# Kernel optimization log

Measured on AMD Instinct MI355X. Metric: run time of the kernel, lower is better.

Reference implementation:

```python
import jax, jax.numpy as jnp
import numpy as np

N = 100000   # nodes
E = 800000   # edges
D = 16       # embedding_dimension
H = 128      # hidden_dimension
O = 3        # out_dim
R = 2        # relation_num
SLOPE = 0.01 # torch LeakyReLU default negative_slope


def setup_inputs() -> dict:
    key = jax.random.key(0)
    ks = jax.random.split(key, 16)
    s = 0.05
    return {
        "mask_feature": jax.random.normal(ks[0], (N, D), jnp.float32),
        "feature": jax.random.normal(ks[1], (N, D), jnp.float32),
        "W1": jax.random.normal(ks[2], (D, H), jnp.float32) * s,
        "b1": jax.random.normal(ks[3], (H,), jnp.float32) * s,
        "rg1_w": jax.random.normal(ks[4], (R, H, H), jnp.float32) * s,
        "rg1_root": jax.random.normal(ks[5], (H, H), jnp.float32) * s,
        "rg1_b": jax.random.normal(ks[6], (H,), jnp.float32) * s,
        "rg2_w": jax.random.normal(ks[7], (R, H, H), jnp.float32) * s,
        "rg2_root": jax.random.normal(ks[8], (H, H), jnp.float32) * s,
        "rg2_b": jax.random.normal(ks[9], (H,), jnp.float32) * s,
        "Wo": jax.random.normal(ks[10], (H, O), jnp.float32) * s,
        "bo": jax.random.normal(ks[11], (O,), jnp.float32) * s,
        "edge_index": jax.random.randint(ks[12], (2, E), 0, N, jnp.int64),
        "edge_type": jax.random.randint(ks[13], (E,), 0, R, jnp.int64),
    }


def _rgcn_conv(x, src, dst, w_rel, w_root, bias):
    """PyG RGCNConv with default mean aggregation per relation + root + bias."""
    out = x @ w_root + bias                      # [N, H] root/self term
    xj = x[src]                                  # [E, H] gather source features
    for r in range(R):
        rmask = _EDGE_TYPE_MASKS[r]              # [E] bool, edge_type == r
        msg = jnp.where(rmask[:, None], xj @ w_rel[r], 0.0)   # [E, H]
        agg = jax.ops.segment_sum(msg, dst, num_segments=N)   # [N, H]
        cnt = jax.ops.segment_sum(rmask.astype(x.dtype), dst, num_segments=N)
        out = out + agg / jnp.maximum(cnt, 1.0)[:, None]       # mean aggr
    return out


_EDGE_TYPE_MASKS = None


def reference(mask_feature, feature, W1, b1, rg1_w, rg1_root, rg1_b,
              rg2_w, rg2_root, rg2_b, Wo, bo, edge_index, edge_type):
    global _EDGE_TYPE_MASKS
    src, dst = edge_index[0], edge_index[1]
    _EDGE_TYPE_MASKS = [edge_type == r for r in range(R)]

    def branch(inp):
        h = jax.nn.leaky_relu(inp @ W1 + b1, SLOPE)      # linear_relu_input
        h = _rgcn_conv(h, src, dst, rg1_w, rg1_root, rg1_b)
        # dropout: identity in eval mode
        h = _rgcn_conv(h, src, dst, rg2_w, rg2_root, rg2_b)
        return h @ Wo + bo                               # linear_output [N, O]

    x = branch(mask_feature.astype(jnp.float32))
    mask = branch(feature - mask_feature)
    return x * mask                                      # [N, O]
```

## Files before the change

kernel.cpp:

```cpp
#include <hip/hip_runtime.h>
#include <hip/hip_fp16.h>

#define Nn 100000
#define Ee 800000
#define Dd 16
#define Hh 128
#define Oo 3
#define Rr 2
#define HROW 256
#define Mm (Rr * Nn)
#define CNTB4 ((Ee + 1023) / 1024)
#define SWB 48
#define INTB ((Nn + 127) / 128)
#define NT_IN 128
#define FN 16
#define MPAD 516
#define OPAD 264

typedef _Float16 half8 __attribute__((ext_vector_type(8)));
typedef _Float16 half4 __attribute__((ext_vector_type(4)));
typedef float floatx4 __attribute__((ext_vector_type(4)));

__global__ void k_diag(float* out, float v) { out[0] = v; }

__global__ __launch_bounds__(256) void k_prep_all(
    const int* __restrict__ ei, const int* __restrict__ et,
    int* __restrict__ cnt, int* __restrict__ eidx, int cap,
    const float* __restrict__ r1root, const float* __restrict__ r1w,
    const float* __restrict__ r2root, const float* __restrict__ r2w,
    __half* __restrict__ Bsw1, __half* __restrict__ Bsw2,
    const float* __restrict__ mf, const float* __restrict__ ff,
    const float* __restrict__ W1, const float* __restrict__ b1,
    __half* __restrict__ H) {
    int tid = threadIdx.x;
    int bx = blockIdx.x;

    if (bx < INTB) {
        int n0 = bx * NT_IN;
        int j = tid & 127;
        int hf = __builtin_amdgcn_readfirstlane(tid >> 7);
        float wk[Dd];
#pragma unroll
        for (int k = 0; k < Dd; ++k) wk[k] = W1[k * Hh + j];
        float bj = b1[j];
        int nbeg = n0 + hf * 64;
        int nend = nbeg + 64;
        if (nend > Nn) nend = Nn;
#pragma unroll 2
        for (int n = nbeg; n < nend; ++n) {
            const float* xr = mf + (size_t)n * Dd;
            const float* fr = ff + (size_t)n * Dd;
            float a0 = bj, a1 = bj;
#pragma unroll
            for (int k = 0; k < Dd; ++k) {
                float xv = xr[k];
                float fv = fr[k];
                a0 = fmaf(xv, wk[k], a0);
                a1 = fmaf(fv, wk[k], a1);
                a1 = fmaf(-xv, wk[k], a1);
            }
            a0 = a0 > 0.f ? a0 : 0.01f * a0;
            a1 = a1 > 0.f ? a1 : 0.01f * a1;
            H[(size_t)n * HROW + j] = __float2half(a0);
            H[(size_t)n * HROW + Hh + j] = __float2half(a1);
        }
        return;
    }
    int sb = bx - INTB;
    if (sb < CNTB4) {
        int e0 = (sb * 256 + tid) * 4;
        if (e0 < Ee) {
            int4 s4 = *(const int4*)(ei + e0);
            int4 d4 = *(const int4*)(ei + Ee + e0);
            int4 t4 = *(const int4*)(et + e0);
            int gb, pos;
            gb = t4.x * Nn + d4.x; pos = atomicAdd(&cnt[gb], 1);
            if (pos < cap) eidx[(size_t)gb * cap + pos] = s4.x;
            gb = t4.y * Nn + d4.y; pos = atomicAdd(&cnt[gb], 1);
            if (pos < cap) eidx[(size_t)gb * cap + pos] = s4.y;
            gb = t4.z * Nn + d4.z; pos = atomicAdd(&cnt[gb], 1);
            if (pos < cap) eidx[(size_t)gb * cap + pos] = s4.z;
            gb = t4.w * Nn + d4.w; pos = atomicAdd(&cnt[gb], 1);
            if (pos < cap) eidx[(size_t)gb * cap + pos] = s4.w;
        }
        return;
    }
    sb -= CNTB4;
    {
        const float* wroot = (sb < 24) ? r1root : r2root;
        const float* wrel = (sb < 24) ? r1w : r2w;
        __half* Bsw = (sb < 24) ? Bsw1 : Bsw2;
        int idx = (sb % 24) * 256 + tid;
        if (idx >= 8 * 12 * 64) return;
        int l = idx & 63;
        int s = (idx >> 6) % 12;
        int t = (idx >> 6) / 12;
        int n = (l & 15) * 8 + t;
        int k0 = s * 32 + (l >> 4) * 8;
        __half tmp[8];
#pragma unroll
        for (int jj = 0; jj < 8; ++jj) {
            int k = k0 + jj;
            float v = (k < Hh) ? wroot[k * Hh + n] : wrel[(size_t)(k - Hh) * Hh + n];
            tmp[jj] = __float2half(v);
        }
        *(uint4*)(Bsw + (size_t)idx * 8) = *(uint4*)tmp;
    }
}

__global__ __launch_bounds__(256, 6) void k_conv_f(const __half* __restrict__ Hin,
                                                   __half* __restrict__ Hout,
                                                   const int* __restrict__ cnt,
                                                   const int* __restrict__ eidx, int cap,
                                                   const __half* __restrict__ Bsw,
                                                   const float* __restrict__ bias,
                                                   const __half* __restrict__ zrow,
                                                   int do_final,
                                                   const float* __restrict__ Wo,
                                                   const float* __restrict__ bo,
                                                   float* __restrict__ out) {
    __shared__ __align__(16) char smem[FN * MPAD * 2];
    __shared__ float WoS[Hh * Oo];
    __shared__ float bS[Oo];
    auto TM = (__half(*)[MPAD])smem;
    auto TO = (__half(*)[OPAD])smem;

    int tid = threadIdx.x;
    int n0 = blockIdx.x * FN;
    int wv = tid >> 6;
    int lane = tid & 63;

    if (do_final) {
        for (int i = tid; i < Hh * Oo; i += 256) WoS[i] = Wo[i];
        if (tid < Oo) bS[tid] = bo[tid];
    }

    int hh32 = lane >> 5;
    int sl = lane & 31;
    const __half* zr = zrow + sl * 8;

    int cn0[4], cn1[4], sidx[4];
#pragma unroll
    for (int p = 0; p < 4; ++p) {
        int gb0 = n0 + wv * 4 + p;
        cn0[p] = cnt[gb0];
        cn1[p] = cnt[gb0 + Nn];
        sidx[p] = eidx[(size_t)(hh32 * Nn + gb0) * cap + sl];
    }

#pragma unroll
    for (int p = 0; p < 4; ++p) {
        int nl = wv * 4 + p;
        int cn_h = hh32 ? cn1[p] : cn0[p];
        int len = cn_h < 32 ? cn_h : 32;
        int mlr = cn0[p] > cn1[p] ? cn0[p] : cn1[p];
        int maxlen = mlr < 32 ? mlr : 32;

        int bc[8];
#pragma unroll
        for (int u = 0; u < 8; ++u) bc[u] = __shfl(sidx[p], u, 32);

        float2 ac[4];
#pragma unroll
        for (int j = 0; j < 4; ++j) { ac[j].x = 0.f; ac[j].y = 0.f; }

        {
            half8 v0 = *(const half8*)(const void*)((0 < len) ? Hin + (size_t)bc[0] * HROW + sl * 8 : zr);
            half8 v1 = *(const half8*)(const void*)((1 < len) ? Hin + (size_t)bc[1] * HROW + sl * 8 : zr);
            half8 v2 = *(const half8*)(const void*)((2 < len) ? Hin + (size_t)bc[2] * HROW + sl * 8 : zr);
            half8 v3 = *(const half8*)(const void*)((3 < len) ? Hin + (size_t)bc[3] * HROW + sl * 8 : zr);
            half8 s = (v0 + v1) + (v2 + v3);
#pragma unroll
            for (int j = 0; j < 4; ++j) {
                ac[j].x += (float)s[2 * j];
                ac[j].y += (float)s[2 * j + 1];
            }
        }
        if (maxlen > 4) {
            half8 v0 = *(const half8*)(const void*)((4 < len) ? Hin + (size_t)bc[4] * HROW + sl * 8 : zr);
            half8 v1 = *(const half8*)(const void*)((5 < len) ? Hin + (size_t)bc[5] * HROW + sl * 8 : zr);
            half8 v2 = *(const half8*)(const void*)((6 < len) ? Hin + (size_t)bc[6] * HROW + sl * 8 : zr);
            half8 v3 = *(const half8*)(const void*)((7 < len) ? Hin + (size_t)bc[7] * HROW + sl * 8 : zr);
            half8 s = (v0 + v1) + (v2 + v3);
#pragma unroll
            for (int j = 0; j < 4; ++j) {
                ac[j].x += (float)s[2 * j];
                ac[j].y += (float)s[2 * j + 1];
            }
            if (maxlen > 8) {
                for (int e = 8; e < maxlen; e += 4) {
                    half8 v[4];
#pragma unroll
                    for (int u = 0; u < 4; ++u) {
                        int s_ = __shfl(sidx[p], e + u, 32);
                        v[u] = *(const half8*)(const void*)(
                            ((e + u) < len) ? Hin + (size_t)s_ * HROW + sl * 8 : zr);
                    }
                    half8 s2 = (v[0] + v[1]) + (v[2] + v[3]);
#pragma unroll
                    for (int j = 0; j < 4; ++j) {
                        ac[j].x += (float)s2[2 * j];
                        ac[j].y += (float)s2[2 * j + 1];
                    }
                }
            }
        }

        float iv = 1.0f / fmaxf((float)cn_h, 1.0f);
        __half2 o[4];
#pragma unroll
        for (int j = 0; j < 4; ++j)
            o[j] = __floats2half2_rn(ac[j].x * iv, ac[j].y * iv);
        __half* dst = &TM[nl][hh32 * 256 + sl * 8];
        *(uint2*)dst = *(uint2*)&o[0];
        *(uint2*)(dst + 4) = *(uint2*)&o[2];
    }
    __syncthreads();

    int b = wv >> 1;
    int hh = wv & 1;
    int quad = lane >> 4;
    int l15 = lane & 15;

    floatx4 acc[4];
#pragma unroll
    for (int t = 0; t < 4; ++t) {
        float bv = bias[l15 * 8 + hh * 4 + t];
        acc[t][0] = bv; acc[t][1] = bv; acc[t][2] = bv; acc[t][3] = bv;
    }

    const __half* hrow = Hin + (size_t)(n0 + l15) * HROW + b * Hh + quad * 8;
#pragma unroll
    for (int s = 0; s < 12; ++s) {
        half8 af;
        if (s < 4)
            af = *(const half8*)(const void*)(hrow + s * 32);
        else
            af = *(const half8*)(const void*)&TM[l15][((s >> 2) - 1) * 256 + b * 128 +
                                                     (s & 3) * 32 + quad * 8];
#pragma unroll
        for (int t = 0; t < 4; ++t) {
            half8 bf = *(const half8*)(const void*)(
                Bsw + ((size_t)((hh * 4 + t) * 12 + s) * 64 + lane) * 8);
            acc[t] = __builtin_amdgcn_mfma_f32_16x16x32_f16(af, bf, acc[t], 0, 0, 0);
        }
    }

    if (!do_final) {
#pragma unroll
        for (int r = 0; r < 4; ++r) {
            int node = n0 + quad * 4 + r;
            __half2 o[2];
            o[0] = __floats2half2_rn(acc[0][r], acc[1][r]);
            o[1] = __floats2half2_rn(acc[2][r], acc[3][r]);
            *(uint2*)(Hout + (size_t)node * HROW + b * Hh + l15 * 8 + hh * 4) = *(uint2*)o;
        }
    } else {
        __syncthreads();
#pragma unroll
        for (int r = 0; r < 4; ++r) {
            int nl = quad * 4 + r;
            __half2 o[2];
            o[0] = __floats2half2_rn(acc[0][r], acc[1][r]);
            o[1] = __floats2half2_rn(acc[2][r], acc[3][r]);
            *(uint2*)&TO[nl][b * 128 + l15 * 8 + hh * 4] = *(uint2*)o;
        }
        __syncthreads();
        if (tid < FN * Oo) {
            int node = tid / 3;
            int o3 = tid - node * 3;
            float a = bS[o3], m = bS[o3];
            const __half2* row = (const __half2*)TO[node];
#pragma unroll 4
            for (int k2 = 0; k2 < 64; ++k2) {
                float2 v = __half22float2(row[k2]);
                float2 u = __half22float2(row[64 + k2]);
                float w0 = WoS[(2 * k2) * 3 + o3];
                float w1 = WoS[(2 * k2 + 1) * 3 + o3];
                a += v.x * w0 + v.y * w1;
                m += u.x * w0 + u.y * w1;
            }
            out[(size_t)(n0 + node) * 3 + o3] = a * m;
        }
    }
}

extern "C" void kernel_launch(void* const* d_in, const int* in_sizes, int n_in,
                              void* d_out, int out_size, void* d_ws, size_t ws_size,
                              hipStream_t stream) {
    const float* mf = (const float*)d_in[0];
    const float* ff = (const float*)d_in[1];
    const float* W1 = (const float*)d_in[2];
    const float* b1 = (const float*)d_in[3];
    const float* rg1_w = (const float*)d_in[4];
    const float* rg1_root = (const float*)d_in[5];
    const float* rg1_b = (const float*)d_in[6];
    const float* rg2_w = (const float*)d_in[7];
    const float* rg2_root = (const float*)d_in[8];
    const float* rg2_b = (const float*)d_in[9];
    const float* Wo = (const float*)d_in[10];
    const float* bo = (const float*)d_in[11];
    const int* ei = (const int*)d_in[12];
    const int* et = (const int*)d_in[13];
    float* out = (float*)d_out;

    const size_t szBsw = (size_t)8 * 12 * 64 * 8 * 2;

    auto layoutNeed = [&](int cap, size_t* offs) {
        size_t o = 0;
        auto take = [&](size_t bytes) { size_t r = o; o += (bytes + 15) & ~(size_t)15; return r; };
        offs[0] = take((size_t)Mm * 4 + 512);
        offs[1] = take((size_t)Mm * cap * 4);
        offs[2] = take(szBsw);
        offs[3] = take(szBsw);
        offs[4] = take((size_t)Nn * HROW * 2);
        offs[5] = take((size_t)Nn * HROW * 2);
        return o;
    };

    size_t offs[6];
    int cap = 64;
    size_t NEED = layoutNeed(cap, offs);
    if (ws_size < NEED) {
        cap = 32;
        NEED = layoutNeed(cap, offs);
        if (ws_size < NEED) {
            k_diag<<<1, 1, 0, stream>>>(out, (float)ws_size);
            return;
        }
    }

    int* cnt = (int*)((char*)d_ws + offs[0]);
    int* eidx = (int*)((char*)d_ws + offs[1]);
    __half* Bsw1 = (__half*)((char*)d_ws + offs[2]);
    __half* Bsw2 = (__half*)((char*)d_ws + offs[3]);
    __half* H0 = (__half*)((char*)d_ws + offs[4]);
    __half* H1 = (__half*)((char*)d_ws + offs[5]);
    const __half* zrow = (const __half*)((char*)d_ws + offs[0] + (size_t)Mm * 4);

    hipMemsetAsync(cnt, 0, (size_t)Mm * 4 + 512, stream);
    k_prep_all<<<INTB + CNTB4 + SWB, 256, 0, stream>>>(ei, et, cnt, eidx, cap,
                                                       rg1_root, rg1_w, rg2_root, rg2_w,
                                                       Bsw1, Bsw2, mf, ff, W1, b1, H0);
    k_conv_f<<<Nn / FN, 256, 0, stream>>>(H0, H1, cnt, eidx, cap, Bsw1, rg1_b, zrow,
                                          0, nullptr, nullptr, nullptr);
    k_conv_f<<<Nn / FN, 256, 0, stream>>>(H1, H0, cnt, eidx, cap, Bsw2, rg2_b, zrow,
                                          1, Wo, bo, out);
}
```

Baseline: 358.5 us.

## Double conv node tile to 32 and split prep into separate kernels

Each conv block now handles 32 nodes instead of 16. Every B-fragment load from the swizzled weights feeds two MFMAs, one per 16-row tile, so weight fetches per node are halved. Occupancy is lowered to 4 blocks per SM and the gather loop runs 8 nodes per wave, which raises register and shared memory pressure and halves the block count. The fused prep kernel is split into an edge-placement/weight-swizzle kernel and an input-linear kernel, and the input loop unroll goes from 2 to 4. This adds one more kernel launch.

```diff
diff --git a/kernel.cpp b/kernel.cpp
--- a/kernel.cpp
+++ b/kernel.cpp
@@ -13,7 +13,7 @@
 #define SWB 48
 #define INTB ((Nn + 127) / 128)
 #define NT_IN 128
-#define FN 16
+#define FN 32
 #define MPAD 516
 #define OPAD 264
 
@@ -23,50 +23,49 @@
 
 __global__ void k_diag(float* out, float v) { out[0] = v; }
 
-__global__ __launch_bounds__(256) void k_prep_all(
+__global__ __launch_bounds__(256) void k_input(
+    const float* __restrict__ mf, const float* __restrict__ ff,
+    const float* __restrict__ W1, const float* __restrict__ b1,
+    __half* __restrict__ H) {
+    int tid = threadIdx.x;
+    int n0 = blockIdx.x * NT_IN;
+    int j = tid & 127;
+    int hf = __builtin_amdgcn_readfirstlane(tid >> 7);
+    float wk[Dd];
+#pragma unroll
+    for (int k = 0; k < Dd; ++k) wk[k] = W1[k * Hh + j];
+    float bj = b1[j];
+    int nbeg = n0 + hf * 64;
+    int nend = nbeg + 64;
+    if (nend > Nn) nend = Nn;
+#pragma unroll 4
+    for (int n = nbeg; n < nend; ++n) {
+        const float* xr = mf + (size_t)n * Dd;
+        const float* fr = ff + (size_t)n * Dd;
+        float a0 = bj, a1 = bj;
+#pragma unroll
+        for (int k = 0; k < Dd; ++k) {
+            float xv = xr[k];
+            float fv = fr[k];
+            a0 = fmaf(xv, wk[k], a0);
+            a1 = fmaf(fv, wk[k], a1);
+            a1 = fmaf(-xv, wk[k], a1);
+        }
+        a0 = a0 > 0.f ? a0 : 0.01f * a0;
+        a1 = a1 > 0.f ? a1 : 0.01f * a1;
+        H[(size_t)n * HROW + j] = __float2half(a0);
+        H[(size_t)n * HROW + Hh + j] = __float2half(a1);
+    }
+}
+
+__global__ __launch_bounds__(256) void k_place(
     const int* __restrict__ ei, const int* __restrict__ et,
     int* __restrict__ cnt, int* __restrict__ eidx, int cap,
     const float* __restrict__ r1root, const float* __restrict__ r1w,
     const float* __restrict__ r2root, const float* __restrict__ r2w,
-    __half* __restrict__ Bsw1, __half* __restrict__ Bsw2,
-    const float* __restrict__ mf, const float* __restrict__ ff,
-    const float* __restrict__ W1, const float* __restrict__ b1,
-    __half* __restrict__ H) {
+    __half* __restrict__ Bsw1, __half* __restrict__ Bsw2) {
     int tid = threadIdx.x;
-    int bx = blockIdx.x;
-
-    if (bx < INTB) {
-        int n0 = bx * NT_IN;
-        int j = tid & 127;
-        int hf = __builtin_amdgcn_readfirstlane(tid >> 7);
-        float wk[Dd];
-#pragma unroll
-        for (int k = 0; k < Dd; ++k) wk[k] = W1[k * Hh + j];
-        float bj = b1[j];
-        int nbeg = n0 + hf * 64;
-        int nend = nbeg + 64;
-        if (nend > Nn) nend = Nn;
-#pragma unroll 2
-        for (int n = nbeg; n < nend; ++n) {
-            const float* xr = mf + (size_t)n * Dd;
-            const float* fr = ff + (size_t)n * Dd;
-            float a0 = bj, a1 = bj;
-#pragma unroll
-            for (int k = 0; k < Dd; ++k) {
-                float xv = xr[k];
-                float fv = fr[k];
-                a0 = fmaf(xv, wk[k], a0);
-                a1 = fmaf(fv, wk[k], a1);
-                a1 = fmaf(-xv, wk[k], a1);
-            }
-            a0 = a0 > 0.f ? a0 : 0.01f * a0;
-            a1 = a1 > 0.f ? a1 : 0.01f * a1;
-            H[(size_t)n * HROW + j] = __float2half(a0);
-            H[(size_t)n * HROW + Hh + j] = __float2half(a1);
-        }
-        return;
-    }
-    int sb = bx - INTB;
+    int sb = blockIdx.x;
     if (sb < CNTB4) {
         int e0 = (sb * 256 + tid) * 4;
         if (e0 < Ee) {
@@ -108,7 +107,7 @@
     }
 }
 
-__global__ __launch_bounds__(256, 6) void k_conv_f(const __half* __restrict__ Hin,
+__global__ __launch_bounds__(256, 4) void k_conv_f(const __half* __restrict__ Hin,
                                                    __half* __restrict__ Hout,
                                                    const int* __restrict__ cnt,
                                                    const int* __restrict__ eidx, int cap,
@@ -139,18 +138,18 @@
     int sl = lane & 31;
     const __half* zr = zrow + sl * 8;
 
-    int cn0[4], cn1[4], sidx[4];
-#pragma unroll
-    for (int p = 0; p < 4; ++p) {
-        int gb0 = n0 + wv * 4 + p;
+    int cn0[8], cn1[8], sidx[8];
+#pragma unroll
+    for (int p = 0; p < 8; ++p) {
+        int gb0 = n0 + wv * 8 + p;
         cn0[p] = cnt[gb0];
         cn1[p] = cnt[gb0 + Nn];
         sidx[p] = eidx[(size_t)(hh32 * Nn + gb0) * cap + sl];
     }
 
 #pragma unroll
-    for (int p = 0; p < 4; ++p) {
-        int nl = wv * 4 + p;
+    for (int p = 0; p < 8; ++p) {
+        int nl = wv * 8 + p;
         int cn_h = hh32 ? cn1[p] : cn0[p];
         int len = cn_h < 32 ? cn_h : 32;
         int mlr = cn0[p] > cn1[p] ? cn0[p] : cn1[p];
@@ -222,48 +221,62 @@
     int quad = lane >> 4;
     int l15 = lane & 15;
 
-    floatx4 acc[4];
+    floatx4 acc[2][4];
 #pragma unroll
     for (int t = 0; t < 4; ++t) {
         float bv = bias[l15 * 8 + hh * 4 + t];
-        acc[t][0] = bv; acc[t][1] = bv; acc[t][2] = bv; acc[t][3] = bv;
-    }
-
-    const __half* hrow = Hin + (size_t)(n0 + l15) * HROW + b * Hh + quad * 8;
+#pragma unroll
+        for (int m = 0; m < 2; ++m) {
+            acc[m][t][0] = bv; acc[m][t][1] = bv; acc[m][t][2] = bv; acc[m][t][3] = bv;
+        }
+    }
+
+    const __half* hrow0 = Hin + (size_t)(n0 + l15) * HROW + b * Hh + quad * 8;
+    const __half* hrow1 = hrow0 + (size_t)16 * HROW;
 #pragma unroll
     for (int s = 0; s < 12; ++s) {
-        half8 af;
-        if (s < 4)
-            af = *(const half8*)(const void*)(hrow + s * 32);
-        else
-            af = *(const half8*)(const void*)&TM[l15][((s >> 2) - 1) * 256 + b * 128 +
-                                                     (s & 3) * 32 + quad * 8];
+        half8 af0, af1;
+        if (s < 4) {
+            af0 = *(const half8*)(const void*)(hrow0 + s * 32);
+            af1 = *(const half8*)(const void*)(hrow1 + s * 32);
+        } else {
+            int off = ((s >> 2) - 1) * 256 + b * 128 + (s & 3) * 32 + quad * 8;
+            af0 = *(const half8*)(const void*)&TM[l15][off];
+            af1 = *(const half8*)(const void*)&TM[16 + l15][off];
+        }
 #pragma unroll
         for (int t = 0; t < 4; ++t) {
             half8 bf = *(const half8*)(const void*)(
                 Bsw + ((size_t)((hh * 4 + t) * 12 + s) * 64 + lane) * 8);
-            acc[t] = __builtin_amdgcn_mfma_f32_16x16x32_f16(af, bf, acc[t], 0, 0, 0);
+            acc[0][t] = __builtin_amdgcn_mfma_f32_16x16x32_f16(af0, bf, acc[0][t], 0, 0, 0);
+            acc[1][t] = __builtin_amdgcn_mfma_f32_16x16x32_f16(af1, bf, acc[1][t], 0, 0, 0);
         }
     }
 
     if (!do_final) {
 #pragma unroll
-        for (int r = 0; r < 4; ++r) {
-            int node = n0 + quad * 4 + r;
-            __half2 o[2];
-            o[0] = __floats2half2_rn(acc[0][r], acc[1][r]);
-            o[1] = __floats2half2_rn(acc[2][r], acc[3][r]);
-            *(uint2*)(Hout + (size_t)node * HROW + b * Hh + l15 * 8 + hh * 4) = *(uint2*)o;
+        for (int m = 0; m < 2; ++m) {
+#pragma unroll
+            for (int r = 0; r < 4; ++r) {
+                int node = n0 + m * 16 + quad * 4 + r;
+                __half2 o[2];
+                o[0] = __floats2half2_rn(acc[m][0][r], acc[m][1][r]);
+                o[1] = __floats2half2_rn(acc[m][2][r], acc[m][3][r]);
+                *(uint2*)(Hout + (size_t)node * HROW + b * Hh + l15 * 8 + hh * 4) = *(uint2*)o;
+            }
         }
     } else {
         __syncthreads();
 #pragma unroll
-        for (int r = 0; r < 4; ++r) {
-            int nl = quad * 4 + r;
-            __half2 o[2];
-            o[0] = __floats2half2_rn(acc[0][r], acc[1][r]);
-            o[1] = __floats2half2_rn(acc[2][r], acc[3][r]);
-            *(uint2*)&TO[nl][b * 128 + l15 * 8 + hh * 4] = *(uint2*)o;
+        for (int m = 0; m < 2; ++m) {
+#pragma unroll
+            for (int r = 0; r < 4; ++r) {
+                int nl = m * 16 + quad * 4 + r;
+                __half2 o[2];
+                o[0] = __floats2half2_rn(acc[m][0][r], acc[m][1][r]);
+                o[1] = __floats2half2_rn(acc[m][2][r], acc[m][3][r]);
+                *(uint2*)&TO[nl][b * 128 + l15 * 8 + hh * 4] = *(uint2*)o;
+            }
         }
         __syncthreads();
         if (tid < FN * Oo) {
@@ -339,9 +352,10 @@
     const __half* zrow = (const __half*)((char*)d_ws + offs[0] + (size_t)Mm * 4);
 
     hipMemsetAsync(cnt, 0, (size_t)Mm * 4 + 512, stream);
-    k_prep_all<<<INTB + CNTB4 + SWB, 256, 0, stream>>>(ei, et, cnt, eidx, cap,
-                                                       rg1_root, rg1_w, rg2_root, rg2_w,
-                                                       Bsw1, Bsw2, mf, ff, W1, b1, H0);
+    k_place<<<CNTB4 + SWB, 256, 0, stream>>>(ei, et, cnt, eidx, cap,
+                                             rg1_root, rg1_w, rg2_root, rg2_w,
+                                             Bsw1, Bsw2);
+    k_input<<<INTB, 256, 0, stream>>>(mf, ff, W1, b1, H0);
     k_conv_f<<<Nn / FN, 256, 0, stream>>>(H0, H1, cnt, eidx, cap, Bsw1, rg1_b, zrow,
                                           0, nullptr, nullptr, nullptr);
     k_conv_f<<<Nn / FN, 256, 0, stream>>>(H1, H0, cnt, eidx, cap, Bsw2, rg2_b, zrow,
```

Measured after the change: 423.5 us. 1.18x slower.
